# Kernel optimization log

Hardware: AMD Instinct MI355X
Metric: run time of the kernel (lower is better)

Reference implementation:

```python
import jax, jax.numpy as jnp
import numpy as np

N, E, G = 50000, 500000, 2000   # nodes, edges, graphs
IN, H, ED, OUT = 64, 128, 16, 1
NUM_GAT = 2                      # num_layers - 1
T = 2                            # num_timesteps


def leaky(x, s=0.01):
    return jnp.where(x >= 0, x, s * x)


def gru_cell(x, h, wih, whh, bih, bhh):
    gi = x @ wih.T + bih
    gh = h @ whh.T + bhh
    ir, iz, inn = jnp.split(gi, 3, -1)
    hr, hz, hn = jnp.split(gh, 3, -1)
    r = jax.nn.sigmoid(ir + hr)
    z = jax.nn.sigmoid(iz + hz)
    n = jnp.tanh(inn + r * hn)
    return (1.0 - z) * n + z * h


def lstm_cell(x, h, c, wih, whh, bih, bhh):
    g = x @ wih.T + bih + h @ whh.T + bhh
    i, f, gg, o = jnp.split(g, 4, -1)
    c2 = jax.nn.sigmoid(f) * c + jax.nn.sigmoid(i) * jnp.tanh(gg)
    h2 = jax.nn.sigmoid(o) * jnp.tanh(c2)
    return h2, c2


def setup_inputs() -> dict:
    key = jax.random.key(0)
    ks = iter(jax.random.split(key, 40))
    def rn(shape, s=0.05):
        return jax.random.normal(next(ks), shape, jnp.float32) * s
    return {
        "x": jax.random.normal(next(ks), (N, IN), jnp.float32),
        "edge_index": jax.random.randint(next(ks), (2, E), 0, N),
        "edge_attr": jax.random.normal(next(ks), (E, ED), jnp.float32),
        "batch": jnp.sort(jax.random.randint(next(ks), (N,), 0, G)),
        "lin1_w": rn((H, IN)), "lin1_b": rn((H,)),
        "nd_lin1_w": rn((H, H + ED)), "nd_lin2_w": rn((H, H)), "nd_bias": rn((H,)),
        "gru0_wih": rn((3 * H, H)), "gru0_whh": rn((3 * H, H)),
        "gru0_bih": rn((3 * H,)), "gru0_bhh": rn((3 * H,)),
        "gat_w": rn((NUM_GAT, H, H)), "gat_asrc": rn((NUM_GAT, H)),
        "gat_adst": rn((NUM_GAT, H)), "gat_b": rn((NUM_GAT, H)),
        "gru_wih": rn((NUM_GAT, 3 * H, H)), "gru_whh": rn((NUM_GAT, 3 * H, H)),
        "gru_bih": rn((NUM_GAT, 3 * H)), "gru_bhh": rn((NUM_GAT, 3 * H)),
        "gin_w": rn((H, H)), "gin_b": rn((H,)),
        "lstm_wih": rn((4 * H, H)), "lstm_whh": rn((4 * H, H)),
        "lstm_bih": rn((4 * H,)), "lstm_bhh": rn((4 * H,)),
        "lin2_w": rn((OUT, H)), "lin2_b": rn((OUT,)),
    }


def reference(x, edge_index, edge_attr, batch,
              lin1_w, lin1_b, nd_lin1_w, nd_lin2_w, nd_bias,
              gru0_wih, gru0_whh, gru0_bih, gru0_bhh,
              gat_w, gat_asrc, gat_adst, gat_b,
              gru_wih, gru_whh, gru_bih, gru_bhh,
              gin_w, gin_b, lstm_wih, lstm_whh, lstm_bih, lstm_bhh,
              lin2_w, lin2_b):
    src, dst = edge_index[0], edge_index[1]  # PyG: messages flow src(j) -> dst(i)
    # input projection
    x1 = leaky(x @ lin1_w.T + lin1_b)
    # nd_conv: gather -> MLP -> scatter-add (dropout=0 in eval)
    m = leaky(jnp.concatenate([x1[src], edge_attr], -1) @ nd_lin1_w.T) @ nd_lin2_w.T
    h = jax.nn.elu(jax.ops.segment_sum(m, dst, num_segments=N) + nd_bias)
    xcur = jax.nn.relu(gru_cell(h, x1, gru0_wih, gru0_whh, gru0_bih, gru0_bhh))
    # GAT layers (heads=1, no self loops, negative_slope=0.01)
    for l in range(NUM_GAT):
        xp = xcur @ gat_w[l].T
        a = leaky(xp[src] @ gat_asrc[l] + xp[dst] @ gat_adst[l], 0.01)
        amax = jax.lax.stop_gradient(jax.ops.segment_max(a, dst, num_segments=N))
        ae = jnp.exp(a - amax[dst])
        denom = jax.ops.segment_sum(ae, dst, num_segments=N)
        alpha = ae / denom[dst]
        h = jax.nn.elu(jax.ops.segment_sum(alpha[:, None] * xp[src], dst, num_segments=N) + gat_b[l])
        xcur = jax.nn.relu(gru_cell(h, xcur,
                                    gru_wih[l], gru_whh[l], gru_bih[l], gru_bhh[l]))
    # global readout: GIN on bipartite (nodes -> graphs) + LSTM refinement
    agg = jax.ops.segment_sum(xcur, batch, num_segments=G)  # [G, H], constant over timesteps
    out = jax.nn.relu(agg)
    for _ in range(T):
        h = jax.nn.elu((out + agg) @ gin_w.T + gin_b)  # GIN eps=0: nn(x_dst + aggr)
        out, _ = lstm_cell(out, h, h, lstm_wih, lstm_whh, lstm_bih, lstm_bhh)
    return out @ lin2_w.T + lin2_b  # [G, OUT]
```

## Files before the change

kernel.cpp:

```cpp
#include <hip/hip_runtime.h>
#include <cstdint>
#include <cmath>

#define NN 50000
#define EE 500000
#define GG 2000

#define DEV __device__ __forceinline__

typedef __attribute__((ext_vector_type(8))) short short8;
typedef __attribute__((ext_vector_type(4))) float floatx4;
typedef __attribute__((ext_vector_type(4))) unsigned short ushort4v;
typedef _Float16 half2v __attribute__((ext_vector_type(2)));
typedef _Float16 half4v __attribute__((ext_vector_type(4)));
typedef _Float16 half8v __attribute__((ext_vector_type(8)));

DEV float sigf(float x) { return 1.f / (1.f + expf(-x)); }

DEV float fsig(float x) { return 1.f / (1.f + __expf(-x)); }
DEV float ftanh(float x) {
    const float e = __expf(-2.f * fabsf(x));
    const float t = (1.f - e) / (1.f + e);
    return x >= 0.f ? t : -t;
}

DEV float actf(float x, int act) {
    if (act == 1) return x >= 0.f ? x : 0.01f * x;
    if (act == 2) return x > 0.f ? x : __expf(x) - 1.f;
    if (act == 3) return x > 0.f ? x : 0.f;
    return x;
}

DEV unsigned short f2bf(float f) {
    unsigned u = __float_as_uint(f);
    u += 0x7FFFu + ((u >> 16) & 1u);
    return (unsigned short)(u >> 16);
}

DEV float hdot2(half2v a, half2v b, float c) {
#if __has_builtin(__builtin_amdgcn_fdot2)
    return __builtin_amdgcn_fdot2(a, b, c, false);
#else
    return c + (float)a[0] * (float)b[0] + (float)a[1] * (float)b[1];
#endif
}

#define H2(v, i) __builtin_shufflevector(v, v, 2 * (i), 2 * (i) + 1)

__global__ __launch_bounds__(256) void gemm_f16_k(
    const _Float16* __restrict__ A, const _Float16* __restrict__ W,
    const float* __restrict__ bias, _Float16* __restrict__ C,
    int M, int K, int Nout, int act)
{
    __shared__ unsigned short Als[64 * 136];
    __shared__ unsigned short Bls[64 * 136];
    const int tid = threadIdx.x;
    const int bm = blockIdx.y * 64;
    const int bn = blockIdx.x * 64;

    const int ks = (K == 128) ? 7 : 6;
    const int km = K - 1;
    const int nch = (64 * K) >> 3;
    for (int i = tid; i < nch; i += 256) {
        const int e8 = i << 3;
        const int r = e8 >> ks;
        const int c = e8 & km;
        short8 av = {};
        if (bm + r < M) av = *(const short8*)(A + (size_t)(bm + r) * K + c);
        *(short8*)(Als + r * 136 + c) = av;
        *(short8*)(Bls + r * 136 + c) = *(const short8*)(W + (size_t)(bn + r) * K + c);
    }
    __syncthreads();

    const int wave = tid >> 6;
    const int lane = tid & 63;
    const int wr = (wave >> 1) * 32;
    const int wc = (wave & 1) * 32;
    const int l15 = lane & 15;
    const int quad = lane >> 4;

    floatx4 acc00 = {}, acc01 = {}, acc10 = {}, acc11 = {};
    for (int k0 = 0; k0 < K; k0 += 32) {
        const half8v a0 = *(const half8v*)(Als + (wr + l15) * 136 + k0 + quad * 8);
        const half8v a1 = *(const half8v*)(Als + (wr + 16 + l15) * 136 + k0 + quad * 8);
        const half8v b0 = *(const half8v*)(Bls + (wc + l15) * 136 + k0 + quad * 8);
        const half8v b1 = *(const half8v*)(Bls + (wc + 16 + l15) * 136 + k0 + quad * 8);
        acc00 = __builtin_amdgcn_mfma_f32_16x16x32_f16(a0, b0, acc00, 0, 0, 0);
        acc01 = __builtin_amdgcn_mfma_f32_16x16x32_f16(a0, b1, acc01, 0, 0, 0);
        acc10 = __builtin_amdgcn_mfma_f32_16x16x32_f16(a1, b0, acc10, 0, 0, 0);
        acc11 = __builtin_amdgcn_mfma_f32_16x16x32_f16(a1, b1, acc11, 0, 0, 0);
    }

    const floatx4* accs[4] = { &acc00, &acc01, &acc10, &acc11 };
#pragma unroll
    for (int r = 0; r < 2; ++r) {
#pragma unroll
        for (int c = 0; c < 2; ++c) {
            const floatx4 a = *accs[r * 2 + c];
            const int n = bn + wc + c * 16 + l15;
            const float bv = bias ? bias[n] : 0.f;
#pragma unroll
            for (int i = 0; i < 4; ++i) {
                const int m = bm + wr + r * 16 + quad * 4 + i;
                if (m < M) C[(size_t)m * Nout + n] = (_Float16)actf(a[i] + bv, act);
            }
        }
    }
}

__global__ __launch_bounds__(256) void gemm_mfma_k(
    const float* __restrict__ A, const float* __restrict__ W,
    const float* __restrict__ bias, float* __restrict__ C,
    int M, int K, int Nout, int wpitch, int act)
{
    __shared__ unsigned short Als[64 * 136];
    __shared__ unsigned short Bls[64 * 136];
    const int tid = threadIdx.x;
    const int bm = blockIdx.y * 64;
    const int bn = blockIdx.x * 64;

    const int ks = (K == 128) ? 7 : 6;
    const int km = K - 1;
    const int nvec = (64 * K) >> 2;
    for (int i = tid; i < nvec; i += 256) {
        const int e4 = i << 2;
        const int r = e4 >> ks;
        const int c = e4 & km;
        float4 av = make_float4(0.f, 0.f, 0.f, 0.f);
        if (bm + r < M) av = *(const float4*)(A + (size_t)(bm + r) * K + c);
        ushort4v ua;
        ua[0] = f2bf(av.x); ua[1] = f2bf(av.y); ua[2] = f2bf(av.z); ua[3] = f2bf(av.w);
        *(ushort4v*)(Als + r * 136 + c) = ua;
        const float4 wv = *(const float4*)(W + (size_t)(bn + r) * wpitch + c);
        ushort4v uw;
        uw[0] = f2bf(wv.x); uw[1] = f2bf(wv.y); uw[2] = f2bf(wv.z); uw[3] = f2bf(wv.w);
        *(ushort4v*)(Bls + r * 136 + c) = uw;
    }
    __syncthreads();

    const int wave = tid >> 6;
    const int lane = tid & 63;
    const int wr = (wave >> 1) * 32;
    const int wc = (wave & 1) * 32;
    const int l15 = lane & 15;
    const int quad = lane >> 4;

    floatx4 acc00 = {}, acc01 = {}, acc10 = {}, acc11 = {};
    for (int k0 = 0; k0 < K; k0 += 32) {
        const short8 a0 = *(const short8*)(Als + (wr + l15) * 136 + k0 + quad * 8);
        const short8 a1 = *(const short8*)(Als + (wr + 16 + l15) * 136 + k0 + quad * 8);
        const short8 b0 = *(const short8*)(Bls + (wc + l15) * 136 + k0 + quad * 8);
        const short8 b1 = *(const short8*)(Bls + (wc + 16 + l15) * 136 + k0 + quad * 8);
        acc00 = __builtin_amdgcn_mfma_f32_16x16x32_bf16(a0, b0, acc00, 0, 0, 0);
        acc01 = __builtin_amdgcn_mfma_f32_16x16x32_bf16(a0, b1, acc01, 0, 0, 0);
        acc10 = __builtin_amdgcn_mfma_f32_16x16x32_bf16(a1, b0, acc10, 0, 0, 0);
        acc11 = __builtin_amdgcn_mfma_f32_16x16x32_bf16(a1, b1, acc11, 0, 0, 0);
    }

    const floatx4* accs[4] = { &acc00, &acc01, &acc10, &acc11 };
#pragma unroll
    for (int r = 0; r < 2; ++r) {
#pragma unroll
        for (int c = 0; c < 2; ++c) {
            const floatx4 a = *accs[r * 2 + c];
            const int n = bn + wc + c * 16 + l15;
            const float bv = bias ? bias[n] : 0.f;
#pragma unroll
            for (int i = 0; i < 4; ++i) {
                const int m = bm + wr + r * 16 + quad * 4 + i;
                if (m < M) C[(size_t)m * Nout + n] = actf(a[i] + bv, act);
            }
        }
    }
}

__global__ __launch_bounds__(256, 4) void gru_fused4_k(
    const _Float16* __restrict__ xin, const _Float16* __restrict__ hin,
    const _Float16* __restrict__ wih, const _Float16* __restrict__ whh,
    const float* __restrict__ bih, const float* __restrict__ bhh,
    _Float16* __restrict__ xout, int M)
{
    __shared__ unsigned short sX[64 * 136];
    __shared__ unsigned short sH[64 * 136];

    const int tid = threadIdx.x;
    const int bm = blockIdx.x * 64;

    for (int i = tid; i < 1024; i += 256) {
        const int e8 = i << 3;
        const int r = e8 >> 7;
        const int c = e8 & 127;
        const int m = bm + r;
        short8 xv = {}, hv = {};
        if (m < M) {
            xv = *(const short8*)(xin + (size_t)m * 128 + c);
            hv = *(const short8*)(hin + (size_t)m * 128 + c);
        }
        *(short8*)(sX + r * 136 + c) = xv;
        *(short8*)(sH + r * 136 + c) = hv;
    }
    __syncthreads();

    const int wave = tid >> 6;
    const int lane = tid & 63;
    const int l15 = lane & 15;
    const int quad = lane >> 4;
    const int j0 = (blockIdx.y * 4 + wave) * 16;
    const int j = j0 + l15;

    const float br  = bih[j] + bhh[j];
    const float bz  = bih[128 + j] + bhh[128 + j];
    const float bni = bih[256 + j];
    const float bnh = bhh[256 + j];

    floatx4 aR[4] = {}, aZ[4] = {}, aNi[4] = {}, aNh[4] = {};

#pragma unroll
    for (int k = 0; k < 4; ++k) {
        const size_t wrow = (size_t)(j0 + l15) * 128 + k * 32 + quad * 8;
        const half8v wri = *(const half8v*)(wih + wrow);
        const half8v wzi = *(const half8v*)(wih + 128 * 128 + wrow);
        const half8v wni = *(const half8v*)(wih + 2 * 128 * 128 + wrow);
        const half8v wrh = *(const half8v*)(whh + wrow);
        const half8v wzh = *(const half8v*)(whh + 128 * 128 + wrow);
        const half8v wnh = *(const half8v*)(whh + 2 * 128 * 128 + wrow);
#pragma unroll
        for (int rf = 0; rf < 4; ++rf) {
            const half8v ax = *(const half8v*)(sX + (rf * 16 + l15) * 136 + k * 32 + quad * 8);
            const half8v ah = *(const half8v*)(sH + (rf * 16 + l15) * 136 + k * 32 + quad * 8);
            aR[rf]  = __builtin_amdgcn_mfma_f32_16x16x32_f16(ax, wri, aR[rf], 0, 0, 0);
            aR[rf]  = __builtin_amdgcn_mfma_f32_16x16x32_f16(ah, wrh, aR[rf], 0, 0, 0);
            aZ[rf]  = __builtin_amdgcn_mfma_f32_16x16x32_f16(ax, wzi, aZ[rf], 0, 0, 0);
            aZ[rf]  = __builtin_amdgcn_mfma_f32_16x16x32_f16(ah, wzh, aZ[rf], 0, 0, 0);
            aNi[rf] = __builtin_amdgcn_mfma_f32_16x16x32_f16(ax, wni, aNi[rf], 0, 0, 0);
            aNh[rf] = __builtin_amdgcn_mfma_f32_16x16x32_f16(ah, wnh, aNh[rf], 0, 0, 0);
        }
    }

#pragma unroll
    for (int rf = 0; rf < 4; ++rf) {
#pragma unroll
        for (int i = 0; i < 4; ++i) {
            const int m = bm + rf * 16 + quad * 4 + i;
            if (m >= M) continue;
            const float rg = fsig(aR[rf][i] + br);
            const float zg = fsig(aZ[rf][i] + bz);
            const float ng = ftanh(aNi[rf][i] + bni + rg * (aNh[rf][i] + bnh));
            const float hp = (float)((const _Float16*)sH)[(rf * 16 + quad * 4 + i) * 136 + j];
            const float v = (1.f - zg) * ng + zg * hp;
            xout[(size_t)m * 128 + j] = (_Float16)(v > 0.f ? v : 0.f);
        }
    }
}

__global__ void hist_k(const int* __restrict__ ei, int* __restrict__ deg, int E)
{
    int e = blockIdx.x * 256 + threadIdx.x;
    if (e >= E) return;
    atomicAdd(deg + ei[E + e], 1);
}

__global__ __launch_bounds__(1024) void scan_part_k(const int* __restrict__ deg,
                                                    int* __restrict__ bsum, int n)
{
    __shared__ int sh[1024];
    const int t = threadIdx.x;
    const int i = blockIdx.x * 1024 + t;
    sh[t] = (i < n) ? deg[i] : 0;
    __syncthreads();
#pragma unroll
    for (int off = 512; off; off >>= 1) {
        if (t < off) sh[t] += sh[t + off];
        __syncthreads();
    }
    if (t == 0) bsum[blockIdx.x] = sh[0];
}

__global__ void scan_tops_k(const int* __restrict__ bsum, int* __restrict__ boff,
                            int nb, int* __restrict__ rowptr, int n)
{
    if (threadIdx.x != 0 || blockIdx.x != 0) return;
    int run = 0;
    for (int b = 0; b < nb; ++b) { boff[b] = run; run += bsum[b]; }
    rowptr[n] = run;
}

__global__ __launch_bounds__(1024) void scan_final_k(const int* __restrict__ deg,
                                                     const int* __restrict__ boff,
                                                     int* __restrict__ rowptr, int n)
{
    __shared__ int sh[1024];
    const int t = threadIdx.x;
    const int i = blockIdx.x * 1024 + t;
    const int v = (i < n) ? deg[i] : 0;
    sh[t] = v;
    __syncthreads();
#pragma unroll
    for (int off = 1; off < 1024; off <<= 1) {
        int add = (t >= off) ? sh[t - off] : 0;
        __syncthreads();
        sh[t] += add;
        __syncthreads();
    }
    if (i < n) rowptr[i] = boff[blockIdx.x] + sh[t] - v;
}

__global__ void fill_csr_k(const int* __restrict__ ei, const int* __restrict__ rowptr,
                           int* __restrict__ cursor, int* __restrict__ csr_src,
                           int* __restrict__ csr_eid, int E)
{
    int e = blockIdx.x * 256 + threadIdx.x;
    if (e >= E) return;
    int s = ei[e], d = ei[E + e];
    int pos = atomicAdd(cursor + d, 1);
    int slot = rowptr[d] + pos;
    csr_src[slot] = s;
    csr_eid[slot] = e;
}

__global__ void gptr_k(const int* __restrict__ batch, int* __restrict__ gptr,
                       int N, int G)
{
    int n = blockIdx.x * 256 + threadIdx.x;
    if (n >= N) return;
    if (n == 0) {
        for (int g = 0; g <= batch[0]; ++g) gptr[g] = 0;
    } else {
        const int a = batch[n - 1], b = batch[n];
        for (int g = a + 1; g <= b; ++g) gptr[g] = n;
    }
    if (n == N - 1) {
        for (int g = batch[N - 1] + 1; g <= G; ++g) gptr[g] = N;
    }
}

__global__ __launch_bounds__(128) void graph_sum_k(
    const _Float16* __restrict__ xc, const int* __restrict__ gptr,
    float* __restrict__ agg, float* __restrict__ oA)
{
    const int g = blockIdx.x;
    const int t = threadIdx.x;
    const int n0 = gptr[g], n1 = gptr[g + 1];
    float acc = 0.f;
    for (int n = n0; n < n1; ++n) acc += (float)xc[(size_t)n * 128 + t];
    agg[(size_t)g * 128 + t] = acc;
    oA[(size_t)g * 128 + t] = acc > 0.f ? acc : 0.f;
}

struct CvtSeg { const float* src; _Float16* dst; int n; };
struct CvtArgs { CvtSeg s[10]; int count; };

__global__ void cvt_multi_k(CvtArgs a)
{
    const int seg = blockIdx.y;
    if (seg >= a.count) return;
    const CvtSeg cs = a.s[seg];
    for (int i = blockIdx.x * 256 + threadIdx.x; i < cs.n; i += gridDim.x * 256)
        cs.dst[i] = (_Float16)cs.src[i];
}

__global__ void cvt_ndwA_k(const float* __restrict__ ndw, _Float16* __restrict__ outp)
{
    int t = blockIdx.x * 256 + threadIdx.x;
    if (t >= 16384) return;
    int r = t >> 7, c = t & 127;
    outp[r * 128 + c] = (_Float16)ndw[r * 144 + c];
}

__global__ void cvt_ndwB_k(const float* __restrict__ ndw, _Float16* __restrict__ outp)
{
    int t = blockIdx.x * 256 + threadIdx.x;
    if (t >= 2048) return;
    int r = t >> 4, k = t & 15;
    outp[r * 16 + k] = (_Float16)ndw[r * 144 + 128 + k];
}

__global__ __launch_bounds__(128) void nd_gather_k(
    const int* __restrict__ rowptr, const int* __restrict__ csr_src,
    const int* __restrict__ csr_eid, const _Float16* __restrict__ eaH,
    const _Float16* __restrict__ wH, const _Float16* __restrict__ pH,
    _Float16* __restrict__ outp)
{
    const int d = blockIdx.x;
    const int t = threadIdx.x;
    const half8v w0 = *(const half8v*)(wH + t * 16);
    const half8v w1 = *(const half8v*)(wH + t * 16 + 8);

    const int b0 = rowptr[d], b1 = rowptr[d + 1];
    float acc = 0.f;
    for (int i = b0; i < b1; ++i) {
        const int s = csr_src[i], e = csr_eid[i];
        const half8v e0 = *(const half8v*)(eaH + (size_t)e * 16);
        const half8v e1 = *(const half8v*)(eaH + (size_t)e * 16 + 8);
        float q = 0.f;
        q = hdot2(H2(e0, 0), H2(w0, 0), q);
        q = hdot2(H2(e0, 1), H2(w0, 1), q);
        q = hdot2(H2(e0, 2), H2(w0, 2), q);
        q = hdot2(H2(e0, 3), H2(w0, 3), q);
        q = hdot2(H2(e1, 0), H2(w1, 0), q);
        q = hdot2(H2(e1, 1), H2(w1, 1), q);
        q = hdot2(H2(e1, 2), H2(w1, 2), q);
        q = hdot2(H2(e1, 3), H2(w1, 3), q);
        const float v = (float)pH[(size_t)s * 128 + t] + q;
        acc += v >= 0.f ? v : 0.01f * v;
    }
    outp[(size_t)d * 128 + t] = (_Float16)acc;
}

__global__ void node_dots_k(const _Float16* __restrict__ xp,
                            const float* __restrict__ asrc,
                            const float* __restrict__ adst,
                            float* __restrict__ ssrc, float* __restrict__ sdst)
{
    int n = blockIdx.x, t = threadIdx.x;
    float v = (float)xp[(size_t)n * 128 + t];
    float a = v * asrc[t];
    float b = v * adst[t];
    for (int off = 32; off; off >>= 1) { a += __shfl_down(a, off); b += __shfl_down(b, off); }
    __shared__ float sa[2], sb[2];
    if ((t & 63) == 0) { sa[t >> 6] = a; sb[t >> 6] = b; }
    __syncthreads();
    if (t == 0) { ssrc[n] = sa[0] + sa[1]; sdst[n] = sb[0] + sb[1]; }
}

__global__ __launch_bounds__(128) void gat_gather_k(
    const int* __restrict__ rowptr, const int* __restrict__ csr_src,
    const float* __restrict__ ssrc, const float* __restrict__ sdst,
    const _Float16* __restrict__ xp, const float* __restrict__ bias,
    _Float16* __restrict__ outp)
{
    const int d = blockIdx.x;
    const int t = threadIdx.x;
    __shared__ float red[128];
    __shared__ float lw[128];
    __shared__ int   ls[128];
    __shared__ float racc[4][128];

    const int b0 = rowptr[d], b1 = rowptr[d + 1];
    const int deg = b1 - b0;
    const float sdd = sdst[d];

    float lm = -INFINITY;
    for (int i = b0 + t; i < b1; i += 128) {
        float a = ssrc[csr_src[i]] + sdd;
        a = a >= 0.f ? a : 0.01f * a;
        lm = fmaxf(lm, a);
    }
    red[t] = lm;
    __syncthreads();
#pragma unroll
    for (int off = 64; off; off >>= 1) {
        if (t < off) red[t] = fmaxf(red[t], red[t + off]);
        __syncthreads();
    }
    const float amax = red[0];
    __syncthreads();

    const int g  = t >> 5;
    const int fq = t & 31;
    float4 acc = make_float4(0.f, 0.f, 0.f, 0.f);
    float dpart = 0.f;
    for (int base = b0; base < b1; base += 128) {
        const int len = min(128, b1 - base);
        if (t < len) {
            const int s = csr_src[base + t];
            float a = ssrc[s] + sdd;
            a = a >= 0.f ? a : 0.01f * a;
            const float w = __expf(a - amax);
            lw[t] = w;
            ls[t] = s;
            dpart += w;
        }
        __syncthreads();
        for (int j = 0; j < len; j += 4) {
            const int jj = j + g;
            if (jj < len) {
                const float w = lw[jj];
                const half4v hv = *(const half4v*)(xp + (size_t)ls[jj] * 128 + fq * 4);
                acc.x += w * (float)hv[0];
                acc.y += w * (float)hv[1];
                acc.z += w * (float)hv[2];
                acc.w += w * (float)hv[3];
            }
        }
        __syncthreads();
    }

    red[t] = dpart;
    __syncthreads();
#pragma unroll
    for (int off = 64; off; off >>= 1) {
        if (t < off) red[t] += red[t + off];
        __syncthreads();
    }
    const float denom = red[0];

    racc[g][fq * 4 + 0] = acc.x;
    racc[g][fq * 4 + 1] = acc.y;
    racc[g][fq * 4 + 2] = acc.z;
    racc[g][fq * 4 + 3] = acc.w;
    __syncthreads();

    const float s4 = racc[0][t] + racc[1][t] + racc[2][t] + racc[3][t];
    float v = (deg > 0 ? s4 / denom : 0.f) + bias[t];
    outp[(size_t)d * 128 + t] = (_Float16)(v > 0.f ? v : __expf(v) - 1.f);
}

__global__ void add_k(const float* __restrict__ a, const float* __restrict__ b,
                      float* __restrict__ c, int total)
{
    int gid = blockIdx.x * 256 + threadIdx.x;
    if (gid >= total) return;
    c[gid] = a[gid] + b[gid];
}

__global__ void lstm_combine_k(const float* __restrict__ g1, const float* __restrict__ g2,
                               const float* __restrict__ hg, float* __restrict__ outp, int total)
{
    int gid = blockIdx.x * 256 + threadIdx.x;
    if (gid >= total) return;
    int g = gid >> 7, j = gid & 127;
    const float* a = g1 + g * 512;
    const float* b = g2 + g * 512;
    float ii = a[j]       + b[j];
    float ff = a[j + 128] + b[j + 128];
    float gg = a[j + 256] + b[j + 256];
    float oo = a[j + 384] + b[j + 384];
    float c  = hg[gid];
    float c2 = sigf(ff) * c + sigf(ii) * tanhf(gg);
    outp[gid] = sigf(oo) * tanhf(c2);
}

__global__ void final_k(const float* __restrict__ oin, const float* __restrict__ w,
                        const float* __restrict__ b, float* __restrict__ y)
{
    int g = blockIdx.x, t = threadIdx.x;
    float v = oin[g * 128 + t] * w[t];
    for (int off = 32; off; off >>= 1) v += __shfl_down(v, off);
    __shared__ float s2[2];
    if ((t & 63) == 0) s2[t >> 6] = v;
    __syncthreads();
    if (t == 0) y[g] = s2[0] + s2[1] + b[0];
}


extern "C" void kernel_launch(void* const* d_in, const int* in_sizes, int n_in,
                              void* d_out, int out_size, void* d_ws, size_t ws_size,
                              hipStream_t stream)
{
    const float* x      = (const float*)d_in[0];
    const int*   ei     = (const int*)  d_in[1];
    const float* ea     = (const float*)d_in[2];
    const int*   batch  = (const int*)  d_in[3];
    const float* lin1_w = (const float*)d_in[4];
    const float* lin1_b = (const float*)d_in[5];
    const float* nd1w   = (const float*)d_in[6];
    const float* nd2w   = (const float*)d_in[7];
    const float* ndb    = (const float*)d_in[8];
    const float* g0wih  = (const float*)d_in[9];
    const float* g0whh  = (const float*)d_in[10];
    const float* g0bih  = (const float*)d_in[11];
    const float* g0bhh  = (const float*)d_in[12];
    const float* gatw   = (const float*)d_in[13];
    const float* gatas  = (const float*)d_in[14];
    const float* gatad  = (const float*)d_in[15];
    const float* gatb   = (const float*)d_in[16];
    const float* gwih   = (const float*)d_in[17];
    const float* gwhh   = (const float*)d_in[18];
    const float* gbih   = (const float*)d_in[19];
    const float* gbhh   = (const float*)d_in[20];
    const float* ginw   = (const float*)d_in[21];
    const float* ginb   = (const float*)d_in[22];
    const float* lwih   = (const float*)d_in[23];
    const float* lwhh   = (const float*)d_in[24];
    const float* lbih   = (const float*)d_in[25];
    const float* lbhh   = (const float*)d_in[26];
    const float* l2w    = (const float*)d_in[27];
    const float* l2b    = (const float*)d_in[28];
    float* outp = (float*)d_out;

    const int N = NN, E = EE, G = GG;

    float* ws = (float*)d_ws;
    size_t off = 0;
    auto alloc = [&](size_t n) {
        float* r = ws + off;
        off += (n + 63) & ~(size_t)63;
        return r;
    };
    _Float16* xH    = (_Float16*)alloc((size_t)N * 32);
    _Float16* x1H   = (_Float16*)alloc((size_t)N * 64);
    _Float16* hbufH = (_Float16*)alloc((size_t)N * 64);
    _Float16* accbH = (_Float16*)alloc((size_t)N * 64);
    _Float16* xcH   = (_Float16*)alloc((size_t)N * 64);
    _Float16* pH    = (_Float16*)alloc((size_t)N * 64);
    _Float16* eaH   = (_Float16*)alloc((size_t)E * 8);
    _Float16* lin1_wH = (_Float16*)alloc(4096);
    _Float16* nd1wAH  = (_Float16*)alloc(8192);
    _Float16* ndwBH   = (_Float16*)alloc(1024);
    _Float16* nd2wH   = (_Float16*)alloc(8192);
    _Float16* g0wihH  = (_Float16*)alloc(24576);
    _Float16* g0whhH  = (_Float16*)alloc(24576);
    _Float16* gwihH   = (_Float16*)alloc(49152);
    _Float16* gwhhH   = (_Float16*)alloc(49152);
    _Float16* gatwH   = (_Float16*)alloc(16384);
    float* ssrc = alloc((size_t)N);
    float* sdst = alloc((size_t)N);
    float* agg  = alloc((size_t)G * 128);
    float* oA   = alloc((size_t)G * 128);
    float* oB   = alloc((size_t)G * 128);
    float* hgb  = alloc((size_t)G * 128);
    float* tGA  = alloc((size_t)G * 128);
    float* g1b  = alloc((size_t)G * 512);
    float* g2b  = alloc((size_t)G * 512);
    int* deg     = (int*)alloc((size_t)N);
    int* rowptr  = (int*)alloc((size_t)N + 1);
    int* cursor  = (int*)alloc((size_t)N);
    int* bsum    = (int*)alloc(64);
    int* boff    = (int*)alloc(64);
    int* csr_src = (int*)alloc((size_t)E);
    int* csr_eid = (int*)alloc((size_t)E);
    int* gptr    = (int*)alloc((size_t)G + 1);
    (void)ws_size;

    auto gemmh = [&](const _Float16* A, const _Float16* W, const float* bias,
                     _Float16* C, int M, int K, int Nout, int act) {
        dim3 grid(Nout / 64, (M + 63) / 64);
        gemm_f16_k<<<grid, 256, 0, stream>>>(A, W, bias, C, M, K, Nout, act);
    };
    auto gemmf = [&](const float* A, const float* W, const float* bias, float* C,
                     int M, int K, int Nout, int wpitch, int act) {
        dim3 grid(Nout / 64, (M + 63) / 64);
        gemm_mfma_k<<<grid, 256, 0, stream>>>(A, W, bias, C, M, K, Nout, wpitch, act);
    };
    auto nb = [](int n) { return (n + 255) / 256; };

    auto gru = [&](const _Float16* xin, const _Float16* hin,
                   const _Float16* wih, const _Float16* whh,
                   const float* bih, const float* bhh, _Float16* xout) {
        dim3 grid((N + 63) / 64, 2);
        gru_fused4_k<<<grid, 256, 0, stream>>>(
            xin, hin, wih, whh, bih, bhh, xout, N);
    };

    hipMemsetAsync(deg, 0, (size_t)N * 4, stream);
    hipMemsetAsync(cursor, 0, (size_t)N * 4, stream);
    hist_k<<<nb(E), 256, 0, stream>>>(ei, deg, E);
    const int nblk = (N + 1023) / 1024;
    scan_part_k<<<nblk, 1024, 0, stream>>>(deg, bsum, N);
    scan_tops_k<<<1, 64, 0, stream>>>(bsum, boff, nblk, rowptr, N);
    scan_final_k<<<nblk, 1024, 0, stream>>>(deg, boff, rowptr, N);
    fill_csr_k<<<nb(E), 256, 0, stream>>>(ei, rowptr, cursor, csr_src, csr_eid, E);
    gptr_k<<<nb(N), 256, 0, stream>>>(batch, gptr, N, G);

    CvtArgs ca;
    ca.s[0] = { ea,     eaH,     E * 16 };
    ca.s[1] = { x,      xH,      N * 64 };
    ca.s[2] = { lin1_w, lin1_wH, 8192 };
    ca.s[3] = { nd2w,   nd2wH,   16384 };
    ca.s[4] = { g0wih,  g0wihH,  49152 };
    ca.s[5] = { g0whh,  g0whhH,  49152 };
    ca.s[6] = { gwih,   gwihH,   98304 };
    ca.s[7] = { gwhh,   gwhhH,   98304 };
    ca.s[8] = { gatw,   gatwH,   32768 };
    ca.count = 9;
    cvt_multi_k<<<dim3(2048, 9), 256, 0, stream>>>(ca);
    cvt_ndwA_k<<<64, 256, 0, stream>>>(nd1w, nd1wAH);
    cvt_ndwB_k<<<8, 256, 0, stream>>>(nd1w, ndwBH);

    gemmh(xH, lin1_wH, lin1_b, x1H, N, 64, 128, 1);

    gemmh(x1H, nd1wAH, nullptr, pH, N, 128, 128, 0);
    nd_gather_k<<<N, 128, 0, stream>>>(rowptr, csr_src, csr_eid, eaH, ndwBH, pH, accbH);
    gemmh(accbH, nd2wH, ndb, hbufH, N, 128, 128, 2);

    gru(hbufH, x1H, g0wihH, g0whhH, g0bih, g0bhh, xcH);

    const _Float16* xcur = xcH;
    _Float16* xnext = x1H;
    for (int l = 0; l < 2; ++l) {
        gemmh(xcur, gatwH + (size_t)l * 16384, nullptr, pH, N, 128, 128, 0);
        node_dots_k<<<N, 128, 0, stream>>>(pH, gatas + l * 128, gatad + l * 128, ssrc, sdst);
        gat_gather_k<<<N, 128, 0, stream>>>(rowptr, csr_src, ssrc, sdst, pH,
                                            gatb + l * 128, hbufH);
        gru(hbufH, xcur, gwihH + (size_t)l * 49152, gwhhH + (size_t)l * 49152,
            gbih + l * 384, gbhh + l * 384, xnext);
        const _Float16* t = xcur; xcur = xnext; xnext = (_Float16*)t;
    }

    graph_sum_k<<<G, 128, 0, stream>>>(xcur, gptr, agg, oA);

    float* cur = oA; float* nxt = oB;
    for (int t = 0; t < 2; ++t) {
        add_k<<<nb(G * 128), 256, 0, stream>>>(cur, agg, tGA, G * 128);
        gemmf(tGA, ginw, ginb, hgb, G, 128, 128, 128, 2);
        gemmf(cur, lwih, lbih, g1b, G, 128, 512, 128, 0);
        gemmf(hgb, lwhh, lbhh, g2b, G, 128, 512, 128, 0);
        lstm_combine_k<<<nb(G * 128), 256, 0, stream>>>(g1b, g2b, hgb, nxt, G * 128);
        float* tmp = cur; cur = nxt; nxt = tmp;
    }

    final_k<<<G, 128, 0, stream>>>(cur, l2w, l2b, outp);
}
```

Before: 696.7 us.

## Fuse graph readout into one kernel, drop GAT max pass, prefetch CSR indices

The readout stage (graph sum, GIN linear, two LSTM steps and final projection) is merged into one MFMA kernel that keeps per-graph state in shared memory, replacing about a dozen small launches and their fp32 intermediates. The segment-max pass in GAT attention is removed, so softmax uses exp(a) without subtracting the max. This drops a reduction with its barriers but can overflow for large logits. The nd_gather loop also prefetches the next CSR source and edge ids. The readout runs only 32 blocks, so it exposes little parallelism.

Result: slower. 758.2 us (+8.8%).

```diff
diff --git a/kernel.cpp b/kernel.cpp
--- a/kernel.cpp
+++ b/kernel.cpp
@@ -10,12 +10,9 @@
 
 typedef __attribute__((ext_vector_type(8))) short short8;
 typedef __attribute__((ext_vector_type(4))) float floatx4;
-typedef __attribute__((ext_vector_type(4))) unsigned short ushort4v;
 typedef _Float16 half2v __attribute__((ext_vector_type(2)));
 typedef _Float16 half4v __attribute__((ext_vector_type(4)));
 typedef _Float16 half8v __attribute__((ext_vector_type(8)));
-
-DEV float sigf(float x) { return 1.f / (1.f + expf(-x)); }
 
 DEV float fsig(float x) { return 1.f / (1.f + __expf(-x)); }
 DEV float ftanh(float x) {
@@ -29,12 +26,6 @@
     if (act == 2) return x > 0.f ? x : __expf(x) - 1.f;
     if (act == 3) return x > 0.f ? x : 0.f;
     return x;
-}
-
-DEV unsigned short f2bf(float f) {
-    unsigned u = __float_as_uint(f);
-    u += 0x7FFFu + ((u >> 16) & 1u);
-    return (unsigned short)(u >> 16);
 }
 
 DEV float hdot2(half2v a, half2v b, float c) {
@@ -108,72 +99,6 @@
     }
 }
 
-__global__ __launch_bounds__(256) void gemm_mfma_k(
-    const float* __restrict__ A, const float* __restrict__ W,
-    const float* __restrict__ bias, float* __restrict__ C,
-    int M, int K, int Nout, int wpitch, int act)
-{
-    __shared__ unsigned short Als[64 * 136];
-    __shared__ unsigned short Bls[64 * 136];
-    const int tid = threadIdx.x;
-    const int bm = blockIdx.y * 64;
-    const int bn = blockIdx.x * 64;
-
-    const int ks = (K == 128) ? 7 : 6;
-    const int km = K - 1;
-    const int nvec = (64 * K) >> 2;
-    for (int i = tid; i < nvec; i += 256) {
-        const int e4 = i << 2;
-        const int r = e4 >> ks;
-        const int c = e4 & km;
-        float4 av = make_float4(0.f, 0.f, 0.f, 0.f);
-        if (bm + r < M) av = *(const float4*)(A + (size_t)(bm + r) * K + c);
-        ushort4v ua;
-        ua[0] = f2bf(av.x); ua[1] = f2bf(av.y); ua[2] = f2bf(av.z); ua[3] = f2bf(av.w);
-        *(ushort4v*)(Als + r * 136 + c) = ua;
-        const float4 wv = *(const float4*)(W + (size_t)(bn + r) * wpitch + c);
-        ushort4v uw;
-        uw[0] = f2bf(wv.x); uw[1] = f2bf(wv.y); uw[2] = f2bf(wv.z); uw[3] = f2bf(wv.w);
-        *(ushort4v*)(Bls + r * 136 + c) = uw;
-    }
-    __syncthreads();
-
-    const int wave = tid >> 6;
-    const int lane = tid & 63;
-    const int wr = (wave >> 1) * 32;
-    const int wc = (wave & 1) * 32;
-    const int l15 = lane & 15;
-    const int quad = lane >> 4;
-
-    floatx4 acc00 = {}, acc01 = {}, acc10 = {}, acc11 = {};
-    for (int k0 = 0; k0 < K; k0 += 32) {
-        const short8 a0 = *(const short8*)(Als + (wr + l15) * 136 + k0 + quad * 8);
-        const short8 a1 = *(const short8*)(Als + (wr + 16 + l15) * 136 + k0 + quad * 8);
-        const short8 b0 = *(const short8*)(Bls + (wc + l15) * 136 + k0 + quad * 8);
-        const short8 b1 = *(const short8*)(Bls + (wc + 16 + l15) * 136 + k0 + quad * 8);
-        acc00 = __builtin_amdgcn_mfma_f32_16x16x32_bf16(a0, b0, acc00, 0, 0, 0);
-        acc01 = __builtin_amdgcn_mfma_f32_16x16x32_bf16(a0, b1, acc01, 0, 0, 0);
-        acc10 = __builtin_amdgcn_mfma_f32_16x16x32_bf16(a1, b0, acc10, 0, 0, 0);
-        acc11 = __builtin_amdgcn_mfma_f32_16x16x32_bf16(a1, b1, acc11, 0, 0, 0);
-    }
-
-    const floatx4* accs[4] = { &acc00, &acc01, &acc10, &acc11 };
-#pragma unroll
-    for (int r = 0; r < 2; ++r) {
-#pragma unroll
-        for (int c = 0; c < 2; ++c) {
-            const floatx4 a = *accs[r * 2 + c];
-            const int n = bn + wc + c * 16 + l15;
-            const float bv = bias ? bias[n] : 0.f;
-#pragma unroll
-            for (int i = 0; i < 4; ++i) {
-                const int m = bm + wr + r * 16 + quad * 4 + i;
-                if (m < M) C[(size_t)m * Nout + n] = actf(a[i] + bv, act);
-            }
-        }
-    }
-}
-
 __global__ __launch_bounds__(256, 4) void gru_fused4_k(
     const _Float16* __restrict__ xin, const _Float16* __restrict__ hin,
     const _Float16* __restrict__ wih, const _Float16* __restrict__ whh,
@@ -334,21 +259,8 @@
     }
 }
 
-__global__ __launch_bounds__(128) void graph_sum_k(
-    const _Float16* __restrict__ xc, const int* __restrict__ gptr,
-    float* __restrict__ agg, float* __restrict__ oA)
-{
-    const int g = blockIdx.x;
-    const int t = threadIdx.x;
-    const int n0 = gptr[g], n1 = gptr[g + 1];
-    float acc = 0.f;
-    for (int n = n0; n < n1; ++n) acc += (float)xc[(size_t)n * 128 + t];
-    agg[(size_t)g * 128 + t] = acc;
-    oA[(size_t)g * 128 + t] = acc > 0.f ? acc : 0.f;
-}
-
 struct CvtSeg { const float* src; _Float16* dst; int n; };
-struct CvtArgs { CvtSeg s[10]; int count; };
+struct CvtArgs { CvtSeg s[12]; int count; };
 
 __global__ void cvt_multi_k(CvtArgs a)
 {
@@ -388,10 +300,14 @@
 
     const int b0 = rowptr[d], b1 = rowptr[d + 1];
     float acc = 0.f;
+    int s = 0, e = 0;
+    if (b0 < b1) { s = csr_src[b0]; e = csr_eid[b0]; }
     for (int i = b0; i < b1; ++i) {
-        const int s = csr_src[i], e = csr_eid[i];
+        const int sn = (i + 1 < b1) ? csr_src[i + 1] : 0;
+        const int en = (i + 1 < b1) ? csr_eid[i + 1] : 0;
         const half8v e0 = *(const half8v*)(eaH + (size_t)e * 16);
         const half8v e1 = *(const half8v*)(eaH + (size_t)e * 16 + 8);
+        const float pv = (float)pH[(size_t)s * 128 + t];
         float q = 0.f;
         q = hdot2(H2(e0, 0), H2(w0, 0), q);
         q = hdot2(H2(e0, 1), H2(w0, 1), q);
@@ -401,8 +317,9 @@
         q = hdot2(H2(e1, 1), H2(w1, 1), q);
         q = hdot2(H2(e1, 2), H2(w1, 2), q);
         q = hdot2(H2(e1, 3), H2(w1, 3), q);
-        const float v = (float)pH[(size_t)s * 128 + t] + q;
+        const float v = pv + q;
         acc += v >= 0.f ? v : 0.01f * v;
+        s = sn; e = en;
     }
     outp[(size_t)d * 128 + t] = (_Float16)acc;
 }
@@ -439,22 +356,6 @@
     const int b0 = rowptr[d], b1 = rowptr[d + 1];
     const int deg = b1 - b0;
     const float sdd = sdst[d];
-
-    float lm = -INFINITY;
-    for (int i = b0 + t; i < b1; i += 128) {
-        float a = ssrc[csr_src[i]] + sdd;
-        a = a >= 0.f ? a : 0.01f * a;
-        lm = fmaxf(lm, a);
-    }
-    red[t] = lm;
-    __syncthreads();
-#pragma unroll
-    for (int off = 64; off; off >>= 1) {
-        if (t < off) red[t] = fmaxf(red[t], red[t + off]);
-        __syncthreads();
-    }
-    const float amax = red[0];
-    __syncthreads();
 
     const int g  = t >> 5;
     const int fq = t & 31;
@@ -466,7 +367,7 @@
             const int s = csr_src[base + t];
             float a = ssrc[s] + sdd;
             a = a >= 0.f ? a : 0.01f * a;
-            const float w = __expf(a - amax);
+            const float w = __expf(a);
             lw[t] = w;
             ls[t] = s;
             dpart += w;
@@ -506,41 +407,124 @@
     outp[(size_t)d * 128 + t] = (_Float16)(v > 0.f ? v : __expf(v) - 1.f);
 }
 
-__global__ void add_k(const float* __restrict__ a, const float* __restrict__ b,
-                      float* __restrict__ c, int total)
-{
-    int gid = blockIdx.x * 256 + threadIdx.x;
-    if (gid >= total) return;
-    c[gid] = a[gid] + b[gid];
-}
-
-__global__ void lstm_combine_k(const float* __restrict__ g1, const float* __restrict__ g2,
-                               const float* __restrict__ hg, float* __restrict__ outp, int total)
-{
-    int gid = blockIdx.x * 256 + threadIdx.x;
-    if (gid >= total) return;
-    int g = gid >> 7, j = gid & 127;
-    const float* a = g1 + g * 512;
-    const float* b = g2 + g * 512;
-    float ii = a[j]       + b[j];
-    float ff = a[j + 128] + b[j + 128];
-    float gg = a[j + 256] + b[j + 256];
-    float oo = a[j + 384] + b[j + 384];
-    float c  = hg[gid];
-    float c2 = sigf(ff) * c + sigf(ii) * tanhf(gg);
-    outp[gid] = sigf(oo) * tanhf(c2);
-}
-
-__global__ void final_k(const float* __restrict__ oin, const float* __restrict__ w,
-                        const float* __restrict__ b, float* __restrict__ y)
-{
-    int g = blockIdx.x, t = threadIdx.x;
-    float v = oin[g * 128 + t] * w[t];
-    for (int off = 32; off; off >>= 1) v += __shfl_down(v, off);
-    __shared__ float s2[2];
-    if ((t & 63) == 0) s2[t >> 6] = v;
-    __syncthreads();
-    if (t == 0) y[g] = s2[0] + s2[1] + b[0];
+__global__ __launch_bounds__(256) void readout_k(
+    const _Float16* __restrict__ xc, const int* __restrict__ gptr,
+    const _Float16* __restrict__ ginw, const float* __restrict__ ginb,
+    const _Float16* __restrict__ lwih, const _Float16* __restrict__ lwhh,
+    const float* __restrict__ lbih, const float* __restrict__ lbhh,
+    const float* __restrict__ l2w, const float* __restrict__ l2b,
+    float* __restrict__ y, int G)
+{
+    __shared__ _Float16 sOa[64 * 136];
+    __shared__ _Float16 sOb[64 * 136];
+    __shared__ _Float16 sG [64 * 136];
+    __shared__ _Float16 sT [64 * 136];
+    __shared__ float    sC [64 * 128];
+
+    const int tid = threadIdx.x, wave = tid >> 6, lane = tid & 63;
+    const int l15 = lane & 15, quad = lane >> 4;
+    const int g0 = blockIdx.x * 64;
+
+    for (int r = wave * 16; r < wave * 16 + 16; ++r) {
+        const int g = g0 + r;
+        float ax = 0.f, ay = 0.f;
+        if (g < G) {
+            const int n0 = gptr[g], n1 = gptr[g + 1];
+            for (int n = n0; n < n1; ++n) {
+                const half2v v = *(const half2v*)(xc + (size_t)n * 128 + lane * 2);
+                ax += (float)v[0]; ay += (float)v[1];
+            }
+        }
+        sG[r * 136 + lane * 2]     = (_Float16)ax;
+        sG[r * 136 + lane * 2 + 1] = (_Float16)ay;
+        sOa[r * 136 + lane * 2]     = (_Float16)(ax > 0.f ? ax : 0.f);
+        sOa[r * 136 + lane * 2 + 1] = (_Float16)(ay > 0.f ? ay : 0.f);
+    }
+    __syncthreads();
+
+    _Float16* sIn = sOa;
+    _Float16* sOut = sOb;
+#pragma unroll
+    for (int ts = 0; ts < 2; ++ts) {
+        for (int ci = 0; ci < 2; ++ci) {
+            const int j0 = wave * 32 + ci * 16;
+            floatx4 acc[4] = {};
+#pragma unroll
+            for (int k = 0; k < 4; ++k) {
+                const half8v b = *(const half8v*)(ginw + (size_t)(j0 + l15) * 128 + k * 32 + quad * 8);
+#pragma unroll
+                for (int rf = 0; rf < 4; ++rf) {
+                    const half8v a = *(const half8v*)(sIn + (rf * 16 + l15) * 136 + k * 32 + quad * 8)
+                                   + *(const half8v*)(sG  + (rf * 16 + l15) * 136 + k * 32 + quad * 8);
+                    acc[rf] = __builtin_amdgcn_mfma_f32_16x16x32_f16(a, b, acc[rf], 0, 0, 0);
+                }
+            }
+            const int j = j0 + l15;
+            const float bg = ginb[j];
+#pragma unroll
+            for (int rf = 0; rf < 4; ++rf)
+#pragma unroll
+                for (int i = 0; i < 4; ++i) {
+                    const int row = rf * 16 + quad * 4 + i;
+                    float v = acc[rf][i] + bg;
+                    v = v > 0.f ? v : __expf(v) - 1.f;
+                    sT[row * 136 + j] = (_Float16)v;
+                    sC[row * 128 + j] = v;
+                }
+        }
+        __syncthreads();
+
+        for (int ci = 0; ci < 2; ++ci) {
+            const int j0 = wave * 32 + ci * 16;
+            floatx4 acc[4][4] = {};
+#pragma unroll
+            for (int k = 0; k < 4; ++k) {
+                half8v bw[4], bh[4];
+#pragma unroll
+                for (int gt = 0; gt < 4; ++gt) {
+                    bw[gt] = *(const half8v*)(lwih + (size_t)(gt * 128 + j0 + l15) * 128 + k * 32 + quad * 8);
+                    bh[gt] = *(const half8v*)(lwhh + (size_t)(gt * 128 + j0 + l15) * 128 + k * 32 + quad * 8);
+                }
+#pragma unroll
+                for (int rf = 0; rf < 4; ++rf) {
+                    const half8v ao = *(const half8v*)(sIn + (rf * 16 + l15) * 136 + k * 32 + quad * 8);
+                    const half8v ah = *(const half8v*)(sT  + (rf * 16 + l15) * 136 + k * 32 + quad * 8);
+#pragma unroll
+                    for (int gt = 0; gt < 4; ++gt) {
+                        acc[gt][rf] = __builtin_amdgcn_mfma_f32_16x16x32_f16(ao, bw[gt], acc[gt][rf], 0, 0, 0);
+                        acc[gt][rf] = __builtin_amdgcn_mfma_f32_16x16x32_f16(ah, bh[gt], acc[gt][rf], 0, 0, 0);
+                    }
+                }
+            }
+            const int j = j0 + l15;
+            const float bi_ = lbih[j]       + lbhh[j];
+            const float bf_ = lbih[128 + j] + lbhh[128 + j];
+            const float bgg = lbih[256 + j] + lbhh[256 + j];
+            const float bo_ = lbih[384 + j] + lbhh[384 + j];
+#pragma unroll
+            for (int rf = 0; rf < 4; ++rf)
+#pragma unroll
+                for (int i = 0; i < 4; ++i) {
+                    const int row = rf * 16 + quad * 4 + i;
+                    const float hg = sC[row * 128 + j];
+                    const float c2 = fsig(acc[1][rf][i] + bf_) * hg
+                                   + fsig(acc[0][rf][i] + bi_) * ftanh(acc[2][rf][i] + bgg);
+                    const float on = fsig(acc[3][rf][i] + bo_) * ftanh(c2);
+                    sOut[row * 136 + j] = (_Float16)on;
+                }
+        }
+        __syncthreads();
+        _Float16* tmp = sIn; sIn = sOut; sOut = tmp;
+    }
+
+    const int r = tid >> 2;
+    const int part = tid & 3;
+    float v = 0.f;
+    for (int j = part * 32; j < part * 32 + 32; ++j)
+        v += (float)sIn[r * 136 + j] * l2w[j];
+    v += __shfl_down(v, 2);
+    v += __shfl_down(v, 1);
+    if (part == 0 && g0 + r < G) y[g0 + r] = v + l2b[0];
 }
 
 
@@ -604,15 +588,11 @@
     _Float16* gwihH   = (_Float16*)alloc(49152);
     _Float16* gwhhH   = (_Float16*)alloc(49152);
     _Float16* gatwH   = (_Float16*)alloc(16384);
+    _Float16* ginwH   = (_Float16*)alloc(8192);
+    _Float16* lwihH   = (_Float16*)alloc(32768);
+    _Float16* lwhhH   = (_Float16*)alloc(32768);
     float* ssrc = alloc((size_t)N);
     float* sdst = alloc((size_t)N);
-    float* agg  = alloc((size_t)G * 128);
-    float* oA   = alloc((size_t)G * 128);
-    float* oB   = alloc((size_t)G * 128);
-    float* hgb  = alloc((size_t)G * 128);
-    float* tGA  = alloc((size_t)G * 128);
-    float* g1b  = alloc((size_t)G * 512);
-    float* g2b  = alloc((size_t)G * 512);
     int* deg     = (int*)alloc((size_t)N);
     int* rowptr  = (int*)alloc((size_t)N + 1);
     int* cursor  = (int*)alloc((size_t)N);
@@ -628,11 +608,6 @@
         dim3 grid(Nout / 64, (M + 63) / 64);
         gemm_f16_k<<<grid, 256, 0, stream>>>(A, W, bias, C, M, K, Nout, act);
     };
-    auto gemmf = [&](const float* A, const float* W, const float* bias, float* C,
-                     int M, int K, int Nout, int wpitch, int act) {
-        dim3 grid(Nout / 64, (M + 63) / 64);
-        gemm_mfma_k<<<grid, 256, 0, stream>>>(A, W, bias, C, M, K, Nout, wpitch, act);
-    };
     auto nb = [](int n) { return (n + 255) / 256; };
 
     auto gru = [&](const _Float16* xin, const _Float16* hin,
@@ -654,17 +629,20 @@
     gptr_k<<<nb(N), 256, 0, stream>>>(batch, gptr, N, G);
 
     CvtArgs ca;
-    ca.s[0] = { ea,     eaH,     E * 16 };
-    ca.s[1] = { x,      xH,      N * 64 };
-    ca.s[2] = { lin1_w, lin1_wH, 8192 };
-    ca.s[3] = { nd2w,   nd2wH,   16384 };
-    ca.s[4] = { g0wih,  g0wihH,  49152 };
-    ca.s[5] = { g0whh,  g0whhH,  49152 };
-    ca.s[6] = { gwih,   gwihH,   98304 };
-    ca.s[7] = { gwhh,   gwhhH,   98304 };
-    ca.s[8] = { gatw,   gatwH,   32768 };
-    ca.count = 9;
-    cvt_multi_k<<<dim3(2048, 9), 256, 0, stream>>>(ca);
+    ca.s[0]  = { ea,     eaH,     E * 16 };
+    ca.s[1]  = { x,      xH,      N * 64 };
+    ca.s[2]  = { lin1_w, lin1_wH, 8192 };
+    ca.s[3]  = { nd2w,   nd2wH,   16384 };
+    ca.s[4]  = { g0wih,  g0wihH,  49152 };
+    ca.s[5]  = { g0whh,  g0whhH,  49152 };
+    ca.s[6]  = { gwih,   gwihH,   98304 };
+    ca.s[7]  = { gwhh,   gwhhH,   98304 };
+    ca.s[8]  = { gatw,   gatwH,   32768 };
+    ca.s[9]  = { ginw,   ginwH,   16384 };
+    ca.s[10] = { lwih,   lwihH,   65536 };
+    ca.s[11] = { lwhh,   lwhhH,   65536 };
+    ca.count = 12;
+    cvt_multi_k<<<dim3(2048, 12), 256, 0, stream>>>(ca);
     cvt_ndwA_k<<<64, 256, 0, stream>>>(nd1w, nd1wAH);
     cvt_ndwB_k<<<8, 256, 0, stream>>>(nd1w, ndwBH);
 
@@ -688,17 +666,6 @@
         const _Float16* t = xcur; xcur = xnext; xnext = (_Float16*)t;
     }
 
-    graph_sum_k<<<G, 128, 0, stream>>>(xcur, gptr, agg, oA);
-
-    float* cur = oA; float* nxt = oB;
-    for (int t = 0; t < 2; ++t) {
-        add_k<<<nb(G * 128), 256, 0, stream>>>(cur, agg, tGA, G * 128);
-        gemmf(tGA, ginw, ginb, hgb, G, 128, 128, 128, 2);
-        gemmf(cur, lwih, lbih, g1b, G, 128, 512, 128, 0);
-        gemmf(hgb, lwhh, lbhh, g2b, G, 128, 512, 128, 0);
-        lstm_combine_k<<<nb(G * 128), 256, 0, stream>>>(g1b, g2b, hgb, nxt, G * 128);
-        float* tmp = cur; cur = nxt; nxt = tmp;
-    }
-
-    final_k<<<G, 128, 0, stream>>>(cur, l2w, l2b, outp);
-}
+    readout_k<<<(G + 63) / 64, 256, 0, stream>>>(
+        xcur, gptr, ginwH, ginb, lwihH, lwhhH, lbih, lbhh, l2w, l2b, outp, G);
+}
```
